# Performance work log

Hardware: AMD Instinct MI355X
Metric: run time of the kernel (lower is better)

The kernel has to match this reference:

```python
import jax, jax.numpy as jnp
import numpy as np

B, S, H = 1, 4096, 2048
NH, NKV = 16, 4
HD = H // NH  # 128
GROUPS = NH // NKV


def setup_inputs() -> dict:
    key = jax.random.key(0)
    ks = jax.random.split(key, 5)
    hidden_states = jax.random.normal(ks[0], (B, S, H), dtype=jnp.float32)
    # causal additive mask: 0 on/below diagonal, large negative above
    neg = jnp.finfo(jnp.float32).min
    causal = jnp.where(jnp.tril(jnp.ones((S, S), dtype=bool)), 0.0, neg)
    attention_mask = jnp.broadcast_to(causal, (B, 1, S, S)).astype(jnp.float32)
    sc = 0.02
    Wq = jax.random.normal(ks[1], (H, NH * HD), dtype=jnp.float32) * sc
    Wk = jax.random.normal(ks[2], (H, NKV * HD), dtype=jnp.float32) * sc
    Wv = jax.random.normal(ks[3], (H, NKV * HD), dtype=jnp.float32) * sc
    Wo = jax.random.normal(ks[4], (H, H), dtype=jnp.float32) * sc
    return {"hidden_states": hidden_states, "attention_mask": attention_mask,
            "Wq": Wq, "Wk": Wk, "Wv": Wv, "Wo": Wo}


def reference(hidden_states, attention_mask, Wq, Wk, Wv, Wo):
    b, s, _ = hidden_states.shape
    # projections -> (b, heads, s, hd)
    q = (hidden_states @ Wq).reshape(b, s, NH, HD).transpose(0, 2, 1, 3)
    k = (hidden_states @ Wk).reshape(b, s, NKV, HD).transpose(0, 2, 1, 3)
    v = (hidden_states @ Wv).reshape(b, s, NKV, HD).transpose(0, 2, 1, 3)
    # repeat_kv for GQA: (b, nkv, s, hd) -> (b, nh, s, hd)
    k = jnp.repeat(k, GROUPS, axis=1)
    v = jnp.repeat(v, GROUPS, axis=1)
    scores = jnp.einsum('bhqd,bhkd->bhqk', q, k) / jnp.sqrt(jnp.float32(HD))
    scores = scores + attention_mask
    attn = jax.nn.softmax(scores.astype(jnp.float32), axis=-1).astype(q.dtype)
    out = jnp.einsum('bhqk,bhkd->bhqd', attn, v)
    out = out.transpose(0, 2, 1, 3).reshape(b, s, H)
    return out @ Wo
```

## Files before the change

### kernel.cpp

```cpp
#include <hip/hip_runtime.h>


typedef __bf16 bf16;
typedef float f32x4 __attribute__((ext_vector_type(4)));
typedef bf16 bf16x4 __attribute__((ext_vector_type(4)));
typedef bf16 bf16x8 __attribute__((ext_vector_type(8)));

#define MFMA16(A, B, C) __builtin_amdgcn_mfma_f32_16x16x32_bf16((A), (B), (C), 0, 0, 0)

__device__ __forceinline__ void async16(const bf16* g, bf16* l) {
  __builtin_amdgcn_global_load_lds(
      (const __attribute__((address_space(1))) unsigned int*)g,
      (__attribute__((address_space(3))) unsigned int*)l, 16, 0, 0);
}

__device__ __forceinline__ float exp2v(float x) {
  float r; asm("v_exp_f32 %0, %1" : "=v"(r) : "v"(x)); return r;
}
__device__ __forceinline__ unsigned cvtpk(float a, float b) {
  unsigned r; asm("v_cvt_pk_bf16_f32 %0, %1, %2" : "=v"(r) : "v"(a), "v"(b)); return r;
}

__global__ void cast_bf16_kernel(const float* __restrict__ in,
                                 bf16* __restrict__ out, int n4) {
  int i = blockIdx.x * blockDim.x + threadIdx.x;
  int stride = gridDim.x * blockDim.x;
  for (; i < n4; i += stride) {
    float4 v = ((const float4*)in)[i];
    bf16x4 o = {(bf16)v.x, (bf16)v.y, (bf16)v.z, (bf16)v.w};
    ((bf16x4*)out)[i] = o;
  }
}

__global__ void transpose_cast_kernel(const float* __restrict__ src, int srcCols,
                                      bf16* __restrict__ dst, float scale) {
  __shared__ float t[64][65];
  const int kt = blockIdx.y * 64;
  const int nt = blockIdx.x * 64;
  const int r0 = threadIdx.x >> 4;
  const int c0 = (threadIdx.x & 15) * 4;
#pragma unroll
  for (int i = 0; i < 4; ++i) {
    int r = r0 + i * 16;
    float4 v = *(const float4*)(src + (kt + r) * srcCols + nt + c0);
    t[r][c0 + 0] = v.x; t[r][c0 + 1] = v.y; t[r][c0 + 2] = v.z; t[r][c0 + 3] = v.w;
  }
  __syncthreads();
#pragma unroll
  for (int i = 0; i < 4; ++i) {
    int r = r0 + i * 16;
    bf16x4 b = {(bf16)(t[c0 + 0][r] * scale), (bf16)(t[c0 + 1][r] * scale),
                (bf16)(t[c0 + 2][r] * scale), (bf16)(t[c0 + 3][r] * scale)};
    *(bf16x4*)(dst + (nt + r) * 2048 + kt + c0) = b;
  }
}

template <int MODE>
__global__ __launch_bounds__(256, 2) void gemm_bt(
    const bf16* __restrict__ A, const bf16* __restrict__ BT, int K,
    bf16* __restrict__ Qb, bf16* __restrict__ Kb, bf16* __restrict__ Vt,
    float* __restrict__ Cf) {
  __shared__ bf16 As[128 * 32];
  __shared__ bf16 Bs[128 * 32];
  const int tid = threadIdx.x;
  const int w = tid >> 6, lane = tid & 63, g = lane >> 4, lq = lane & 15;
  const int wr = w >> 1, wc = w & 1;
  const int mBase = blockIdx.y * 128, nBase = blockIdx.x * 128;

  f32x4 acc[4][4] = {};
  const int KT = K >> 5;
  for (int kt = 0; kt < KT; ++kt) {
#pragma unroll
    for (int r = 0; r < 2; ++r) {
      int chunk = r * 256 + tid;
      int row = chunk >> 2, cu = chunk & 3;
      async16(A + (mBase + row) * K + kt * 32 + cu * 8, As + (r * 256 + w * 64) * 8);
      async16(BT + (nBase + row) * K + kt * 32 + cu * 8, Bs + (r * 256 + w * 64) * 8);
    }
    asm volatile("s_waitcnt vmcnt(0)" ::: "memory");
    __syncthreads();

    bf16x8 af[4], bfr[4];
#pragma unroll
    for (int i = 0; i < 4; ++i)
      af[i] = *(const bf16x8*)(As + (wr * 64 + i * 16 + lq) * 32 + g * 8);
#pragma unroll
    for (int i = 0; i < 4; ++i)
      bfr[i] = *(const bf16x8*)(Bs + (wc * 64 + i * 16 + lq) * 32 + g * 8);
#pragma unroll
    for (int mi = 0; mi < 4; ++mi)
#pragma unroll
      for (int ni = 0; ni < 4; ++ni)
        acc[mi][ni] = MFMA16(af[mi], bfr[ni], acc[mi][ni]);
    __syncthreads();
  }

#pragma unroll
  for (int mi = 0; mi < 4; ++mi)
#pragma unroll
    for (int ni = 0; ni < 4; ++ni) {
      const int n = nBase + wc * 64 + ni * 16 + lq;
      const int m0 = mBase + wr * 64 + mi * 16 + 4 * g;
      if (MODE == 0) {
        if (nBase < 2048) {
#pragma unroll
          for (int jr = 0; jr < 4; ++jr)
            Qb[(m0 + jr) * 2048 + n] = (bf16)acc[mi][ni][jr];
        } else if (nBase < 2560) {
#pragma unroll
          for (int jr = 0; jr < 4; ++jr)
            Kb[(m0 + jr) * 512 + (n - 2048)] = (bf16)acc[mi][ni][jr];
        } else {
          bf16x4 v = {(bf16)acc[mi][ni][0], (bf16)acc[mi][ni][1],
                      (bf16)acc[mi][ni][2], (bf16)acc[mi][ni][3]};
          *(bf16x4*)(Vt + (n - 2560) * 4096 + m0) = v;
        }
      } else {
#pragma unroll
        for (int jr = 0; jr < 4; ++jr)
          Cf[(m0 + jr) * 2048 + n] = acc[mi][ni][jr];
      }
    }
}

__global__ __launch_bounds__(256, 2) void attn_fwd(
    const bf16* __restrict__ Qb,
    const bf16* __restrict__ Kb,
    const bf16* __restrict__ Vt,
    bf16* __restrict__ AO) {
  __shared__ __align__(16) bf16 Ks[2][64 * 128];
  __shared__ __align__(16) bf16 Vs[2][128 * 64];

  const int bid = blockIdx.x;
  const int h = bid & 15;
  const int qt = (bid < 256) ? (bid >> 4) : (31 - ((bid - 256) >> 4));
  const int kv = h >> 2;
  const int tid = threadIdx.x;
  const int w = tid >> 6, lane = tid & 63, g = lane >> 4, lq = lane & 15;
  const int sx = (lq & 7) << 4;
  const int qbase = qt * 128;
  const int nk = 2 * (qt + 1);

  bf16x8 aq[2][4];
#pragma unroll
  for (int mi = 0; mi < 2; ++mi)
#pragma unroll
    for (int kk = 0; kk < 4; ++kk)
      aq[mi][kk] = *(const bf16x8*)(Qb + (qbase + w * 32 + mi * 16 + lq) * 2048 +
                                    h * 128 + kk * 32 + g * 8);

  float mst[2] = {-1e30f, -1e30f}, lst[2] = {0.f, 0.f};
  f32x4 o[2][8] = {};

  auto STAGE = [&](int t) {
    const int b = t & 1;
#pragma unroll
    for (int r = 0; r < 4; ++r) {
      int gid = r * 256 + tid;
      int krow = gid >> 4, cu = gid & 15;
      async16(Kb + (t * 64 + krow) * 512 + kv * 128 + ((cu ^ (krow & 7)) * 8),
              &Ks[b][(r * 256 + w * 64) * 8]);
    }
#pragma unroll
    for (int r = 0; r < 4; ++r) {
      int gid = r * 256 + tid;
      int vrow = gid >> 3, gv = gid & 7;
      async16(Vt + (kv * 128 + vrow) * 4096 + t * 64 + ((gv ^ (vrow & 7)) * 8),
              &Vs[b][(r * 256 + w * 64) * 8]);
    }
  };

  STAGE(0);

  for (int t = 0; t < nk; ++t) {
    const int cur = t & 1;
    if (t + 1 < nk) {
      STAGE(t + 1);
      asm volatile("s_waitcnt vmcnt(8)" ::: "memory");
    } else {
      asm volatile("s_waitcnt vmcnt(0)" ::: "memory");
    }
    __builtin_amdgcn_s_barrier();
    __builtin_amdgcn_sched_barrier(0);

    f32x4 s[2][4] = {};
#pragma unroll
    for (int nt = 0; nt < 4; ++nt)
#pragma unroll
      for (int kk = 0; kk < 4; ++kk) {
        bf16x8 bk = *(const bf16x8*)((const char*)Ks[cur] + (nt * 16 + lq) * 256 +
                                     ((kk * 64 + g * 16) ^ sx));
        s[0][nt] = MFMA16(bk, aq[0][kk], s[0][nt]);
        s[1][nt] = MFMA16(bk, aq[1][kk], s[1][nt]);
      }

    if (t >= 2 * qt) {
#pragma unroll
      for (int mi = 0; mi < 2; ++mi) {
        const int q = qbase + w * 32 + mi * 16 + lq;
#pragma unroll
        for (int nt = 0; nt < 4; ++nt)
#pragma unroll
          for (int jr = 0; jr < 4; ++jr) {
            int key = t * 64 + nt * 16 + 4 * g + jr;
            if (key > q) s[mi][nt][jr] = -1e30f;
          }
      }
    }

    unsigned pw[2][4][2];
#pragma unroll
    for (int mi = 0; mi < 2; ++mi) {
      float pm = s[mi][0][0];
#pragma unroll
      for (int nt = 0; nt < 4; ++nt)
#pragma unroll
        for (int jr = 0; jr < 4; ++jr) pm = fmaxf(pm, s[mi][nt][jr]);
      pm = fmaxf(pm, __shfl_xor(pm, 16));
      pm = fmaxf(pm, __shfl_xor(pm, 32));
      if (__any(pm > mst[mi] + 8.f)) {
        float mn = fmaxf(mst[mi], pm);
        float al = exp2v(mst[mi] - mn);
        mst[mi] = mn;
        lst[mi] *= al;
#pragma unroll
        for (int dt = 0; dt < 8; ++dt)
#pragma unroll
          for (int jr = 0; jr < 4; ++jr) o[mi][dt][jr] *= al;
      }
      float rs = 0.f;
      float p[4][4];
#pragma unroll
      for (int nt = 0; nt < 4; ++nt)
#pragma unroll
        for (int jr = 0; jr < 4; ++jr) {
          p[nt][jr] = exp2v(s[mi][nt][jr] - mst[mi]);
          rs += p[nt][jr];
        }
      rs += __shfl_xor(rs, 16);
      rs += __shfl_xor(rs, 32);
      lst[mi] += rs;
#pragma unroll
      for (int nt = 0; nt < 4; ++nt) {
        pw[mi][nt][0] = cvtpk(p[nt][0], p[nt][1]);
        pw[mi][nt][1] = cvtpk(p[nt][2], p[nt][3]);
      }
    }

    const int sg0 = ((g & 1) << 5) + lq;
    const int sg1 = sg0 + 16;
    const bool hi = (g & 2) != 0;
#pragma unroll
    for (int kk2 = 0; kk2 < 2; ++kk2) {
      bf16x8 av[8];
#pragma unroll
      for (int dt = 0; dt < 8; ++dt)
        av[dt] = *(const bf16x8*)((const char*)Vs[cur] + (dt * 16 + lq) * 128 +
                                  ((kk2 * 64 + g * 16) ^ sx));
#pragma unroll
      for (int mi = 0; mi < 2; ++mi) {
        unsigned a0 = __shfl(pw[mi][2 * kk2][0], sg0);
        unsigned a1 = __shfl(pw[mi][2 * kk2 + 1][0], sg0);
        unsigned a2 = __shfl(pw[mi][2 * kk2][1], sg0);
        unsigned a3 = __shfl(pw[mi][2 * kk2 + 1][1], sg0);
        unsigned a4 = __shfl(pw[mi][2 * kk2][0], sg1);
        unsigned a5 = __shfl(pw[mi][2 * kk2 + 1][0], sg1);
        unsigned a6 = __shfl(pw[mi][2 * kk2][1], sg1);
        unsigned a7 = __shfl(pw[mi][2 * kk2 + 1][1], sg1);
        union { unsigned u[4]; bf16x8 v; } pb;
        pb.u[0] = hi ? a1 : a0;
        pb.u[1] = hi ? a3 : a2;
        pb.u[2] = hi ? a5 : a4;
        pb.u[3] = hi ? a7 : a6;
#pragma unroll
        for (int dt = 0; dt < 8; ++dt) o[mi][dt] = MFMA16(av[dt], pb.v, o[mi][dt]);
      }
    }

    __builtin_amdgcn_sched_barrier(0);
    __builtin_amdgcn_s_barrier();
  }

#pragma unroll
  for (int mi = 0; mi < 2; ++mi) {
    const float inv = 1.f / lst[mi];
    const int q = qbase + w * 32 + mi * 16 + lq;
#pragma unroll
    for (int dt = 0; dt < 8; ++dt) {
      bf16x4 ov = {(bf16)(o[mi][dt][0] * inv), (bf16)(o[mi][dt][1] * inv),
                   (bf16)(o[mi][dt][2] * inv), (bf16)(o[mi][dt][3] * inv)};
      *(bf16x4*)(AO + q * 2048 + h * 128 + dt * 16 + 4 * g) = ov;
    }
  }
}

extern "C" void kernel_launch(void* const* d_in, const int* in_sizes, int n_in,
                              void* d_out, int out_size, void* d_ws, size_t ws_size,
                              hipStream_t stream) {
  const float* X = (const float*)d_in[0];
  const float* Wq = (const float*)d_in[2];
  const float* Wk = (const float*)d_in[3];
  const float* Wv = (const float*)d_in[4];
  const float* Wo = (const float*)d_in[5];
  float* out = (float*)d_out;
  char* ws = (char*)d_ws;

  bf16* Xb = (bf16*)ws;
  bf16* WT = (bf16*)(ws + 16777216);
  bf16* Qb = (bf16*)(ws + 29360128);
  bf16* Kb = (bf16*)(ws + 46137344);
  bf16* Vt = (bf16*)(ws + 50331648);

  cast_bf16_kernel<<<2048, 256, 0, stream>>>(X, Xb, (4096 * 2048) / 4);
  transpose_cast_kernel<<<dim3(32, 32), 256, 0, stream>>>(
      Wq, 2048, WT, 0.08838834764831845f * 1.4426950408889634f);
  transpose_cast_kernel<<<dim3(8, 32), 256, 0, stream>>>(Wk, 512, WT + 2048 * 2048, 1.0f);
  transpose_cast_kernel<<<dim3(8, 32), 256, 0, stream>>>(Wv, 512, WT + 2560 * 2048, 1.0f);

  gemm_bt<0><<<dim3(24, 32), 256, 0, stream>>>(Xb, WT, 2048, Qb, Kb, Vt, (float*)nullptr);

  transpose_cast_kernel<<<dim3(32, 32), 256, 0, stream>>>(Wo, 2048, WT, 1.0f);

  attn_fwd<<<512, 256, 0, stream>>>(Qb, Kb, Vt, Xb);

  gemm_bt<1><<<dim3(16, 32), 256, 0, stream>>>(Xb, WT, 2048, (bf16*)nullptr,
                                               (bf16*)nullptr, (bf16*)nullptr, out);
}
```

Baseline: 281.5 us.

## Switch attention kernel to 32x32x16 MFMA with permlane32 swap for P fragments

Rewrites the attention inner loop to use 32x32x16 bf16 MFMA tiles instead of 16x16x32, so each wave holds one 32-row query tile and reduces the softmax row max and row sum mostly within a lane instead of across lanes. The P operand is rebuilt with v_permlane32_swap instead of eight __shfl calls per fragment, and s_setprio is raised around the MFMA blocks. This aims to cut LDS and cross-lane shuffle traffic and give larger MFMA tiles, at the cost of a different register footprint (f32x16 accumulators) and changed LDS read patterns.

Measured after the change: 263.2 us. 1.07x faster.

```diff
diff --git a/kernel.cpp b/kernel.cpp
--- a/kernel.cpp
+++ b/kernel.cpp
@@ -3,10 +3,13 @@
 
 typedef __bf16 bf16;
 typedef float f32x4 __attribute__((ext_vector_type(4)));
+typedef float f32x16 __attribute__((ext_vector_type(16)));
 typedef bf16 bf16x4 __attribute__((ext_vector_type(4)));
 typedef bf16 bf16x8 __attribute__((ext_vector_type(8)));
+typedef unsigned u32x4 __attribute__((ext_vector_type(4)));
 
 #define MFMA16(A, B, C) __builtin_amdgcn_mfma_f32_16x16x32_bf16((A), (B), (C), 0, 0, 0)
+#define MFMA32(A, B, C) __builtin_amdgcn_mfma_f32_32x32x16_bf16((A), (B), (C), 0, 0, 0)
 
 __device__ __forceinline__ void async16(const bf16* g, bf16* l) {
   __builtin_amdgcn_global_load_lds(
@@ -19,6 +22,15 @@
 }
 __device__ __forceinline__ unsigned cvtpk(float a, float b) {
   unsigned r; asm("v_cvt_pk_bf16_f32 %0, %1, %2" : "=v"(r) : "v"(a), "v"(b)); return r;
+}
+#define PLSWAP(a, b) asm("v_permlane32_swap_b32 %0, %1" : "+v"(a), "+v"(b))
+
+__device__ __forceinline__ bf16x8 mkfrag(unsigned a0, unsigned a1,
+                                         unsigned c0, unsigned c1) {
+  PLSWAP(a0, c0);
+  PLSWAP(a1, c1);
+  u32x4 t = {a0, a1, c0, c1};
+  return __builtin_bit_cast(bf16x8, t);
 }
 
 __global__ void cast_bf16_kernel(const float* __restrict__ in,
@@ -136,21 +148,22 @@
   const int qt = (bid < 256) ? (bid >> 4) : (31 - ((bid - 256) >> 4));
   const int kv = h >> 2;
   const int tid = threadIdx.x;
-  const int w = tid >> 6, lane = tid & 63, g = lane >> 4, lq = lane & 15;
-  const int sx = (lq & 7) << 4;
+  const int w = tid >> 6, lane = tid & 63, l5 = lane & 31, g2 = lane >> 5;
+  const int sxr = (l5 & 7) << 4;
   const int qbase = qt * 128;
   const int nk = 2 * (qt + 1);
-
-  bf16x8 aq[2][4];
-#pragma unroll
-  for (int mi = 0; mi < 2; ++mi)
-#pragma unroll
-    for (int kk = 0; kk < 4; ++kk)
-      aq[mi][kk] = *(const bf16x8*)(Qb + (qbase + w * 32 + mi * 16 + lq) * 2048 +
-                                    h * 128 + kk * 32 + g * 8);
-
-  float mst[2] = {-1e30f, -1e30f}, lst[2] = {0.f, 0.f};
-  f32x4 o[2][8] = {};
+  const int qw = qbase + w * 32 + l5;
+
+  bf16x8 aq[8];
+  {
+    const bf16* qrow = Qb + qw * 2048 + h * 128;
+#pragma unroll
+    for (int kk = 0; kk < 8; ++kk)
+      aq[kk] = *(const bf16x8*)(qrow + kk * 16 + g2 * 8);
+  }
+
+  float mst = -1e30f, lst = 0.f;
+  f32x16 o[4] = {};
 
   auto STAGE = [&](int t) {
     const int b = t & 1;
@@ -183,114 +196,110 @@
     __builtin_amdgcn_s_barrier();
     __builtin_amdgcn_sched_barrier(0);
 
-    f32x4 s[2][4] = {};
-#pragma unroll
-    for (int nt = 0; nt < 4; ++nt)
-#pragma unroll
-      for (int kk = 0; kk < 4; ++kk) {
-        bf16x8 bk = *(const bf16x8*)((const char*)Ks[cur] + (nt * 16 + lq) * 256 +
-                                     ((kk * 64 + g * 16) ^ sx));
-        s[0][nt] = MFMA16(bk, aq[0][kk], s[0][nt]);
-        s[1][nt] = MFMA16(bk, aq[1][kk], s[1][nt]);
-      }
+    f32x16 s0 = {}, s1 = {};
+    {
+      const char* kb0 = (const char*)&Ks[cur][0] + l5 * 256;
+      __builtin_amdgcn_s_setprio(1);
+#pragma unroll
+      for (int kk = 0; kk < 8; ++kk) {
+        const int off = (kk * 32 + g2 * 16) ^ sxr;
+        bf16x8 k0 = *(const bf16x8*)(kb0 + off);
+        bf16x8 k1 = *(const bf16x8*)(kb0 + 8192 + off);
+        s0 = MFMA32(k0, aq[kk], s0);
+        s1 = MFMA32(k1, aq[kk], s1);
+      }
+      __builtin_amdgcn_s_setprio(0);
+    }
 
     if (t >= 2 * qt) {
-#pragma unroll
-      for (int mi = 0; mi < 2; ++mi) {
-        const int q = qbase + w * 32 + mi * 16 + lq;
-#pragma unroll
-        for (int nt = 0; nt < 4; ++nt)
-#pragma unroll
-          for (int jr = 0; jr < 4; ++jr) {
-            int key = t * 64 + nt * 16 + 4 * g + jr;
-            if (key > q) s[mi][nt][jr] = -1e30f;
-          }
-      }
-    }
-
-    unsigned pw[2][4][2];
-#pragma unroll
-    for (int mi = 0; mi < 2; ++mi) {
-      float pm = s[mi][0][0];
-#pragma unroll
-      for (int nt = 0; nt < 4; ++nt)
-#pragma unroll
-        for (int jr = 0; jr < 4; ++jr) pm = fmaxf(pm, s[mi][nt][jr]);
-      pm = fmaxf(pm, __shfl_xor(pm, 16));
-      pm = fmaxf(pm, __shfl_xor(pm, 32));
-      if (__any(pm > mst[mi] + 8.f)) {
-        float mn = fmaxf(mst[mi], pm);
-        float al = exp2v(mst[mi] - mn);
-        mst[mi] = mn;
-        lst[mi] *= al;
-#pragma unroll
-        for (int dt = 0; dt < 8; ++dt)
-#pragma unroll
-          for (int jr = 0; jr < 4; ++jr) o[mi][dt][jr] *= al;
-      }
-      float rs = 0.f;
-      float p[4][4];
-#pragma unroll
-      for (int nt = 0; nt < 4; ++nt)
-#pragma unroll
-        for (int jr = 0; jr < 4; ++jr) {
-          p[nt][jr] = exp2v(s[mi][nt][jr] - mst[mi]);
-          rs += p[nt][jr];
-        }
-      rs += __shfl_xor(rs, 16);
-      rs += __shfl_xor(rs, 32);
-      lst[mi] += rs;
-#pragma unroll
-      for (int nt = 0; nt < 4; ++nt) {
-        pw[mi][nt][0] = cvtpk(p[nt][0], p[nt][1]);
-        pw[mi][nt][1] = cvtpk(p[nt][2], p[nt][3]);
-      }
-    }
-
-    const int sg0 = ((g & 1) << 5) + lq;
-    const int sg1 = sg0 + 16;
-    const bool hi = (g & 2) != 0;
-#pragma unroll
-    for (int kk2 = 0; kk2 < 2; ++kk2) {
-      bf16x8 av[8];
-#pragma unroll
-      for (int dt = 0; dt < 8; ++dt)
-        av[dt] = *(const bf16x8*)((const char*)Vs[cur] + (dt * 16 + lq) * 128 +
-                                  ((kk2 * 64 + g * 16) ^ sx));
-#pragma unroll
-      for (int mi = 0; mi < 2; ++mi) {
-        unsigned a0 = __shfl(pw[mi][2 * kk2][0], sg0);
-        unsigned a1 = __shfl(pw[mi][2 * kk2 + 1][0], sg0);
-        unsigned a2 = __shfl(pw[mi][2 * kk2][1], sg0);
-        unsigned a3 = __shfl(pw[mi][2 * kk2 + 1][1], sg0);
-        unsigned a4 = __shfl(pw[mi][2 * kk2][0], sg1);
-        unsigned a5 = __shfl(pw[mi][2 * kk2 + 1][0], sg1);
-        unsigned a6 = __shfl(pw[mi][2 * kk2][1], sg1);
-        unsigned a7 = __shfl(pw[mi][2 * kk2 + 1][1], sg1);
-        union { unsigned u[4]; bf16x8 v; } pb;
-        pb.u[0] = hi ? a1 : a0;
-        pb.u[1] = hi ? a3 : a2;
-        pb.u[2] = hi ? a5 : a4;
-        pb.u[3] = hi ? a7 : a6;
-#pragma unroll
-        for (int dt = 0; dt < 8; ++dt) o[mi][dt] = MFMA16(av[dt], pb.v, o[mi][dt]);
-      }
+      const int kb = t * 64 + 4 * g2;
+#pragma unroll
+      for (int r = 0; r < 16; ++r) {
+        const int key = kb + (r & 3) + 8 * (r >> 2);
+        if (key > qw) s0[r] = -1e30f;
+        if (key + 32 > qw) s1[r] = -1e30f;
+      }
+    }
+
+    {
+      float mx[16];
+#pragma unroll
+      for (int r = 0; r < 16; ++r) mx[r] = fmaxf(s0[r], s1[r]);
+#pragma unroll
+      for (int off = 8; off > 0; off >>= 1)
+#pragma unroll
+        for (int r = 0; r < off; ++r) mx[r] = fmaxf(mx[r], mx[r + off]);
+      const float pm = fmaxf(mx[0], __shfl_xor(mx[0], 32));
+
+      if (__any(pm > mst + 8.f)) {
+        const float mn = fmaxf(mst, pm);
+        const float al = exp2v(mst - mn);
+        mst = mn;
+        lst *= al;
+#pragma unroll
+        for (int dt = 0; dt < 4; ++dt)
+#pragma unroll
+          for (int r = 0; r < 16; ++r) o[dt][r] *= al;
+      }
+#pragma unroll
+      for (int r = 0; r < 16; ++r) {
+        s0[r] = exp2v(s0[r] - mst);
+        s1[r] = exp2v(s1[r] - mst);
+      }
+      float sm[16];
+#pragma unroll
+      for (int r = 0; r < 16; ++r) sm[r] = s0[r] + s1[r];
+#pragma unroll
+      for (int off = 8; off > 0; off >>= 1)
+#pragma unroll
+        for (int r = 0; r < off; ++r) sm[r] += sm[r + off];
+      lst += sm[0] + __shfl_xor(sm[0], 32);
+    }
+
+    unsigned pw0[8], pw1[8];
+#pragma unroll
+    for (int wi = 0; wi < 8; ++wi) {
+      pw0[wi] = cvtpk(s0[2 * wi], s0[2 * wi + 1]);
+      pw1[wi] = cvtpk(s1[2 * wi], s1[2 * wi + 1]);
+    }
+    bf16x8 pb0 = mkfrag(pw0[0], pw0[1], pw0[2], pw0[3]);
+    bf16x8 pb1 = mkfrag(pw0[4], pw0[5], pw0[6], pw0[7]);
+    bf16x8 pb2 = mkfrag(pw1[0], pw1[1], pw1[2], pw1[3]);
+    bf16x8 pb3 = mkfrag(pw1[4], pw1[5], pw1[6], pw1[7]);
+
+    {
+      __builtin_amdgcn_s_setprio(1);
+#pragma unroll
+      for (int dt = 0; dt < 4; ++dt) {
+        const char* vb = (const char*)&Vs[cur][0] + (dt * 32 + l5) * 128;
+        bf16x8 av;
+        av = *(const bf16x8*)(vb + ((0 * 32 + g2 * 16) ^ sxr));
+        o[dt] = MFMA32(av, pb0, o[dt]);
+        av = *(const bf16x8*)(vb + ((1 * 32 + g2 * 16) ^ sxr));
+        o[dt] = MFMA32(av, pb1, o[dt]);
+        av = *(const bf16x8*)(vb + ((2 * 32 + g2 * 16) ^ sxr));
+        o[dt] = MFMA32(av, pb2, o[dt]);
+        av = *(const bf16x8*)(vb + ((3 * 32 + g2 * 16) ^ sxr));
+        o[dt] = MFMA32(av, pb3, o[dt]);
+      }
+      __builtin_amdgcn_s_setprio(0);
     }
 
     __builtin_amdgcn_sched_barrier(0);
     __builtin_amdgcn_s_barrier();
   }
 
-#pragma unroll
-  for (int mi = 0; mi < 2; ++mi) {
-    const float inv = 1.f / lst[mi];
-    const int q = qbase + w * 32 + mi * 16 + lq;
-#pragma unroll
-    for (int dt = 0; dt < 8; ++dt) {
-      bf16x4 ov = {(bf16)(o[mi][dt][0] * inv), (bf16)(o[mi][dt][1] * inv),
-                   (bf16)(o[mi][dt][2] * inv), (bf16)(o[mi][dt][3] * inv)};
-      *(bf16x4*)(AO + q * 2048 + h * 128 + dt * 16 + 4 * g) = ov;
-    }
+  {
+    const float inv = 1.f / lst;
+    bf16* aob = AO + qw * 2048 + h * 128;
+#pragma unroll
+    for (int dt = 0; dt < 4; ++dt)
+#pragma unroll
+      for (int m = 0; m < 4; ++m) {
+        bf16x4 ov = {(bf16)(o[dt][4 * m + 0] * inv), (bf16)(o[dt][4 * m + 1] * inv),
+                     (bf16)(o[dt][4 * m + 2] * inv), (bf16)(o[dt][4 * m + 3] * inv)};
+        *(bf16x4*)(aob + dt * 32 + 8 * m + 4 * g2) = ov;
+      }
   }
 }
 
```
